# Kernel optimization log

Hardware: AMD Instinct MI355X
Metric: run time of the kernel (lower is better)

The kernel has to match this reference:

```python
import jax, jax.numpy as jnp
import numpy as np

# Grid / point-count constants (K-Radar-style sparse voxel grid)
B, Z, Y, X = 4, 40, 1024, 1024
Nr, Nl = 262144, 1048576
W_OCC, W_OFF, W_FEAT = 0.2, 1.0, 1.0
BIG = jnp.int32(1_000_000_000)  # sentinel for unmatched candidates


def _hash_zyx(b, z, y, x):
    # max value B*Z*Y*X ~ 1.7e8, fits int32
    return ((b * Z + z) * Y + y) * X + x


def _make_offsets(R):
    rng = np.arange(-R, R + 1)
    dz, dy, dx = np.meshgrid(rng, rng, rng, indexing='ij')
    return jnp.asarray(np.stack([dz.ravel(), dy.ravel(), dx.ravel()], axis=1), dtype=jnp.int32)  # [K,3]


def setup_inputs() -> dict:
    key = jax.random.key(0)
    k = jax.random.split(key, 10)
    radar_indices = jnp.stack([
        jax.random.randint(k[0], (Nr,), 0, B, dtype=jnp.int32),
        jax.random.randint(k[1], (Nr,), 0, Z, dtype=jnp.int32),
        jax.random.randint(k[2], (Nr,), 0, Y, dtype=jnp.int32),
        jax.random.randint(k[3], (Nr,), 0, X, dtype=jnp.int32)], axis=1)
    lidar_indices = jnp.stack([
        jax.random.randint(k[4], (Nl,), 0, B, dtype=jnp.int32),
        jax.random.randint(k[5], (Nl,), 0, Z, dtype=jnp.int32),
        jax.random.randint(k[6], (Nl,), 0, Y, dtype=jnp.int32),
        jax.random.randint(k[7], (Nl,), 0, X, dtype=jnp.int32)], axis=1)
    pred_feat = jax.random.normal(k[8], (Nr, 4), dtype=jnp.float32)
    pred_occ = jax.random.normal(k[9], (Nr, 1, 1), dtype=jnp.float32)
    lidar_features = jax.random.normal(jax.random.fold_in(key, 77), (Nl, 4), dtype=jnp.float32)
    return {"pred_feat": pred_feat, "pred_occ": pred_occ, "radar_indices": radar_indices,
            "lidar_features": lidar_features, "lidar_indices": lidar_indices, "R": 1}


def _local_match(radar_indices, lidar_indices, lidar_features, R):
    # Build sorted hash table of lidar voxels
    hL = _hash_zyx(lidar_indices[:, 0], lidar_indices[:, 1], lidar_indices[:, 2], lidar_indices[:, 3])
    ordL = jnp.argsort(hL)
    hL_sorted = hL[ordL]

    offs = _make_offsets(R)                      # [K,3]
    K = offs.shape[0]
    b, z, y, x = radar_indices[:, 0], radar_indices[:, 1], radar_indices[:, 2], radar_indices[:, 3]
    zz = jnp.clip(z[:, None] + offs[None, :, 0], 0, Z - 1)   # [Nr,K]
    yy = jnp.clip(y[:, None] + offs[None, :, 1], 0, Y - 1)
    xx = jnp.clip(x[:, None] + offs[None, :, 2], 0, X - 1)
    cand = _hash_zyx(b[:, None], zz, yy, xx).reshape(-1)      # [Nr*K]

    pos = jnp.searchsorted(hL_sorted, cand)                   # [Nr*K]
    safe_pos = jnp.clip(pos, 0, hL_sorted.shape[0] - 1)
    is_member = (pos < hL_sorted.shape[0]) & (hL_sorted[safe_pos] == cand)
    hit = is_member.reshape(-1, K)                            # [Nr,K]

    dL1 = jnp.sum(jnp.abs(offs), axis=1)                      # [K]
    dL1_masked = jnp.where(hit, dL1[None, :], BIG)            # [Nr,K]
    best_k = jnp.argmin(dL1_masked, axis=1)                   # [Nr]
    best = jnp.take_along_axis(dL1_masked, best_k[:, None], axis=1)[:, 0]
    matched = best < BIG                                      # [Nr] bool

    pos_flat = jnp.take_along_axis(pos.reshape(-1, K), best_k[:, None], axis=1)[:, 0]
    lidar_row = ordL[jnp.clip(pos_flat, 0, hL_sorted.shape[0] - 1)]
    gt_feat = jnp.where(matched[:, None], lidar_features[lidar_row], 0.0)  # [Nr, C_lidar]

    sel_z = jnp.take_along_axis(zz, best_k[:, None], axis=1)[:, 0]
    sel_y = jnp.take_along_axis(yy, best_k[:, None], axis=1)[:, 0]
    sel_x = jnp.take_along_axis(xx, best_k[:, None], axis=1)[:, 0]
    gt_offsets = jnp.stack([sel_z - z, sel_y - y, sel_x - x], axis=1).astype(jnp.float32)
    return matched, gt_offsets, gt_feat


def reference(pred_feat, pred_occ, radar_indices, lidar_features, lidar_indices, R):
    matched, gt_d, gt_f = _local_match(radar_indices, lidar_indices, lidar_features, R)
    gt_d = gt_d[:, ::-1]                              # torch.flip(gt_d, dims=[1])
    m = matched.astype(pred_feat.dtype)

    # BCEWithLogitsLoss(mean): logaddexp(0,x) - x*y
    occ_logits = jnp.mean(jnp.squeeze(pred_occ, axis=1), axis=-1)  # [Nr]
    occ_loss = jnp.mean(jnp.logaddexp(0.0, occ_logits) - occ_logits * m)

    cnt = jnp.sum(m)
    # smooth_l1 (beta=1, mean) over matched rows of pred offsets [M,3]
    diff = pred_feat[:, :3] - gt_d
    ad = jnp.abs(diff)
    sl1 = jnp.where(ad < 1.0, 0.5 * diff * diff, ad - 0.5)
    off_loss = jnp.sum(sl1 * m[:, None]) / jnp.maximum(cnt * 3.0, 1.0)
    # l1 (mean) over matched intensity column [M,1]
    feat_loss = jnp.sum(jnp.abs(pred_feat[:, 3:4] - gt_f[:, 3:4]) * m[:, None]) / jnp.maximum(cnt, 1.0)

    return W_OCC * occ_loss + W_OFF * off_loss + W_FEAT * feat_loss
```

## Files before the change

### kernel.cpp

```cpp
#include <hip/hip_runtime.h>
#include <math.h>
#include <limits.h>

#define BD 4
#define ZD 40
#define YD 1024
#define XD 1024
#define BZYX (167772160)

constexpr int BLOCK = 256;
constexpr unsigned SMALL_LOG = 19;
constexpr unsigned long long EMPTY64 = ~0ull;
constexpr size_t OCC_BYTES = (size_t)1 << (SMALL_LOG - 3);

typedef unsigned uvec4 __attribute__((ext_vector_type(4)));

__device__ __forceinline__ unsigned hash_mix(unsigned x) {
    x ^= x >> 16; x *= 0x7feb352dU;
    x ^= x >> 15; x *= 0x846ca68bU;
    x ^= x >> 16;
    return x;
}

__device__ __forceinline__ float smooth_l1(float d) {
    float ad = fabsf(d);
    return (ad < 1.0f) ? 0.5f * d * d : ad - 0.5f;
}

__device__ __forceinline__ float logaddexp0(float logit) {
    return (logit > 0.0f) ? (logit + log1pf(expf(-logit))) : log1pf(expf(logit));
}

__global__ void clear_bitmap(uvec4* __restrict__ bmv, int bmW4) {
    const uvec4 z = (uvec4)(0u);
    const int stride = gridDim.x * blockDim.x;
    for (int k = blockIdx.x * blockDim.x + threadIdx.x; k < bmW4; k += stride)
        bmv[k] = z;
}

__global__ void build_bitmap(const int4* __restrict__ li, int Nl,
                             unsigned* __restrict__ bm,
                             unsigned* __restrict__ cells,
                             uvec4* __restrict__ stv, int stW4) {
    const int gid = blockIdx.x * blockDim.x + threadIdx.x;
    if (gid < Nl) {
        int4 v = li[gid];
        unsigned cell = ((unsigned)(v.x * ZD + v.y) * YD + v.z) * XD + v.w;
        cells[gid] = cell;
        atomicOr(&bm[cell >> 5], 1u << (cell & 31));
    }
    const uvec4 f = (uvec4)(~0u);
    const int stride = gridDim.x * blockDim.x;
    for (int k = gid; k < stW4; k += stride)
        stv[k] = f;
}

__global__ void __launch_bounds__(BLOCK)
main_match(const float4* __restrict__ pf, const float* __restrict__ occ,
           const int4* __restrict__ ri, const unsigned* __restrict__ bm,
           unsigned long long* __restrict__ stab, unsigned* __restrict__ occbm,
           unsigned smask, const int* __restrict__ Rptr, int Nr,
           int* __restrict__ mcell, double* __restrict__ partials) {
    const int R = *Rptr;
    const int i = blockIdx.x * BLOCK + threadIdx.x;
    double occ_s = 0.0, cnt_s = 0.0, off_s = 0.0;

    if (i < Nr) {
        int4 rib = ri[i];
        const int b = rib.x, z = rib.y, y = rib.z, x = rib.w;
        int mc = -1;
        float m = 0.0f;
        int sx = 0, sy = 0, sz = 0;
        bool matched = false;

        if (R == 1) {
            const int xa = max(x - 1, 0);
            const int xc = min(x + 1, XD - 1);
            const int sa = x - xa;
            const int sc = xc - xa;
            unsigned hm = 0;
#pragma unroll
            for (int dz = -1; dz <= 1; ++dz) {
                const int zz = min(max(z + dz, 0), ZD - 1);
#pragma unroll
                for (int dy = -1; dy <= 1; ++dy) {
                    const int yy = min(max(y + dy, 0), YD - 1);
                    const unsigned n0 =
                        ((unsigned)(b * ZD + zz) * YD + yy) * XD + (unsigned)xa;
                    const unsigned q = n0 >> 5;
                    const int r = n0 & 31;
                    unsigned long long w =
                        ((unsigned long long)bm[q + 1] << 32) | bm[q];
                    w >>= r;
                    const int k0 = (dz + 1) * 9 + (dy + 1) * 3;
                    hm |= ((unsigned)(w & 1)) << (k0 + 0);
                    hm |= ((unsigned)((w >> sa) & 1)) << (k0 + 1);
                    hm |= ((unsigned)((w >> sc) & 1)) << (k0 + 2);
                }
            }
            const unsigned M0 = 1u << 13;
            const unsigned M1 = (1u << 4) | (1u << 10) | (1u << 12) |
                                (1u << 14) | (1u << 16) | (1u << 22);
            const unsigned M2 = (1u << 1) | (1u << 3) | (1u << 5) | (1u << 7) |
                                (1u << 9) | (1u << 11) | (1u << 15) | (1u << 17) |
                                (1u << 19) | (1u << 21) | (1u << 23) | (1u << 25);
            int bk = -1;
            if (hm & M0)       bk = 13;
            else if (hm & M1)  bk = __ffs((int)(hm & M1)) - 1;
            else if (hm & M2)  bk = __ffs((int)(hm & M2)) - 1;
            else if (hm)       bk = __ffs((int)hm) - 1;
            if (bk >= 0) {
                matched = true;
                const int dz = bk / 9 - 1, dy = (bk / 3) % 3 - 1, dx = bk % 3 - 1;
                sz = min(max(z + dz, 0), ZD - 1);
                sy = min(max(y + dy, 0), YD - 1);
                sx = min(max(x + dx, 0), XD - 1);
            }
        } else {
            int bestd = INT_MAX;
            for (int dz = -R; dz <= R; ++dz) {
                const int zz = min(max(z + dz, 0), ZD - 1);
                const int adz = abs(dz);
                for (int dy = -R; dy <= R; ++dy) {
                    const int yy = min(max(y + dy, 0), YD - 1);
                    const int adzy = adz + abs(dy);
                    for (int dx = -R; dx <= R; ++dx) {
                        const int d = adzy + abs(dx);
                        if (d >= bestd) continue;
                        const int xx = min(max(x + dx, 0), XD - 1);
                        const unsigned cell =
                            ((unsigned)(b * ZD + zz) * YD + yy) * XD + xx;
                        if ((bm[cell >> 5] >> (cell & 31)) & 1u) {
                            bestd = d; matched = true;
                            sz = zz; sy = yy; sx = xx;
                        }
                    }
                }
            }
        }

        if (matched) {
            m = 1.0f;
            cnt_s = 1.0;
            const unsigned cell = ((unsigned)(b * ZD + sz) * YD + sy) * XD + sx;
            mc = (int)cell;
            const float4 p = pf[i];
            off_s = (double)(smooth_l1(p.x - (float)(sx - x)) +
                             smooth_l1(p.y - (float)(sy - y)) +
                             smooth_l1(p.z - (float)(sz - z)));
            const unsigned long long desired =
                ((unsigned long long)cell << 32) | 0xFFFFFFFFull;
            unsigned s = hash_mix(cell) & smask;
            bool claimed = false;
            while (true) {
                unsigned long long old = atomicCAS(&stab[s], EMPTY64, desired);
                if (old == EMPTY64) { claimed = true; break; }
                if ((unsigned)(old >> 32) == cell) break;
                s = (s + 1) & smask;
            }
            if (claimed) atomicOr(&occbm[s >> 5], 1u << (s & 31));
        }
        mcell[i] = mc;
        const float logit = occ[i];
        occ_s = (double)(logaddexp0(logit) - logit * m);
    }

    __shared__ double sh[3][BLOCK];
    const int tid = threadIdx.x;
    sh[0][tid] = occ_s; sh[1][tid] = cnt_s; sh[2][tid] = off_s;
    __syncthreads();
    for (int s = BLOCK / 2; s > 0; s >>= 1) {
        if (tid < s) {
            sh[0][tid] += sh[0][tid + s];
            sh[1][tid] += sh[1][tid + s];
            sh[2][tid] += sh[2][tid + s];
        }
        __syncthreads();
    }
    if (tid == 0) {
        partials[blockIdx.x * 4 + 0] = sh[0][0];
        partials[blockIdx.x * 4 + 1] = sh[1][0];
        partials[blockIdx.x * 4 + 2] = sh[2][0];
        partials[blockIdx.x * 4 + 3] = 0.0;
    }
}

__global__ void lidar_scan(const unsigned* __restrict__ cells, int Nl,
                           unsigned long long* __restrict__ stab,
                           const unsigned* __restrict__ occbm, unsigned smask) {
    int j = blockIdx.x * blockDim.x + threadIdx.x;
    if (j >= Nl) return;
    const unsigned cell = cells[j];
    unsigned s = hash_mix(cell) & smask;
    if (!((occbm[s >> 5] >> (s & 31)) & 1u)) return;
    while (true) {
        const unsigned long long e = stab[s];
        if (e == EMPTY64) return;
        if ((unsigned)(e >> 32) == cell) {
            atomicMin((unsigned*)&stab[s], (unsigned)j);
            return;
        }
        s = (s + 1) & smask;
    }
}

__global__ void __launch_bounds__(BLOCK)
feat_pass(const float4* __restrict__ pf, const int* __restrict__ mcell,
          const unsigned long long* __restrict__ stab, unsigned smask,
          const float4* __restrict__ lf, int Nr, double* __restrict__ fpart) {
    const int i = blockIdx.x * BLOCK + threadIdx.x;
    double fs = 0.0;
    if (i < Nr) {
        const int mc = mcell[i];
        if (mc >= 0) {
            const unsigned cell = (unsigned)mc;
            unsigned s = hash_mix(cell) & smask;
            unsigned row = 0;
            while (true) {
                const unsigned long long e = stab[s];
                if ((unsigned)(e >> 32) == cell) { row = (unsigned)e; break; }
                s = (s + 1) & smask;
            }
            fs = (double)fabsf(pf[i].w - lf[row].w);
        }
    }
    __shared__ double sh[BLOCK];
    const int tid = threadIdx.x;
    sh[tid] = fs;
    __syncthreads();
    for (int s = BLOCK / 2; s > 0; s >>= 1) {
        if (tid < s) sh[tid] += sh[tid + s];
        __syncthreads();
    }
    if (tid == 0) fpart[blockIdx.x] = sh[0];
}


__global__ void fb_insert(const int4* __restrict__ li, int Nl,
                          unsigned long long* __restrict__ tab, unsigned cmask) {
    int i = blockIdx.x * blockDim.x + threadIdx.x;
    if (i >= Nl) return;
    int4 v = li[i];
    const unsigned cell = ((unsigned)(v.x * ZD + v.y) * YD + v.z) * XD + v.w;
    const unsigned long long desired = ((unsigned long long)cell << 32) | (unsigned)i;
    unsigned s = hash_mix(cell) & cmask;
    unsigned probes = 0;
    while (probes++ <= cmask) {
        const unsigned long long old = atomicCAS(&tab[s], EMPTY64, desired);
        if (old == EMPTY64) return;
        if ((unsigned)(old >> 32) == cell) {
            atomicMin((unsigned*)&tab[s], (unsigned)i);
            return;
        }
        s = (s + 1) & cmask;
    }
}

__global__ void __launch_bounds__(BLOCK)
fb_main(const float4* __restrict__ pf, const float* __restrict__ occ,
        const int4* __restrict__ ri, const float4* __restrict__ lf,
        const unsigned long long* __restrict__ tab, unsigned cmask,
        const int* __restrict__ Rptr, int Nr, double* __restrict__ partials) {
    const int R = *Rptr;
    const int i = blockIdx.x * BLOCK + threadIdx.x;
    double occ_s = 0.0, cnt_s = 0.0, off_s = 0.0, feat_s = 0.0;
    if (i < Nr) {
        int4 rib = ri[i];
        const int b = rib.x, z = rib.y, y = rib.z, x = rib.w;
        int bestd = INT_MAX, bestRow = -1;
        int sx = 0, sy = 0, sz = 0;
        for (int dz = -R; dz <= R; ++dz) {
            const int zz = min(max(z + dz, 0), ZD - 1);
            const int adz = abs(dz);
            for (int dy = -R; dy <= R; ++dy) {
                const int yy = min(max(y + dy, 0), YD - 1);
                const int adzy = adz + abs(dy);
                for (int dx = -R; dx <= R; ++dx) {
                    const int d = adzy + abs(dx);
                    if (d >= bestd) continue;
                    const int xx = min(max(x + dx, 0), XD - 1);
                    const unsigned cell =
                        ((unsigned)(b * ZD + zz) * YD + yy) * XD + xx;
                    unsigned s = hash_mix(cell) & cmask;
                    int row = -1;
                    while (true) {
                        const unsigned long long e = tab[s];
                        if ((unsigned)(e >> 32) == cell) { row = (int)(unsigned)e; break; }
                        if (e == EMPTY64) break;
                        s = (s + 1) & cmask;
                    }
                    if (row >= 0) { bestd = d; bestRow = row; sz = zz; sy = yy; sx = xx; }
                }
            }
        }
        const float m = (bestRow >= 0) ? 1.0f : 0.0f;
        const float logit = occ[i];
        occ_s = (double)(logaddexp0(logit) - logit * m);
        if (bestRow >= 0) {
            cnt_s = 1.0;
            const float4 p = pf[i];
            off_s = (double)(smooth_l1(p.x - (float)(sx - x)) +
                             smooth_l1(p.y - (float)(sy - y)) +
                             smooth_l1(p.z - (float)(sz - z)));
            feat_s = (double)fabsf(p.w - lf[bestRow].w);
        }
    }
    __shared__ double sh[4][BLOCK];
    const int tid = threadIdx.x;
    sh[0][tid] = occ_s; sh[1][tid] = cnt_s; sh[2][tid] = off_s; sh[3][tid] = feat_s;
    __syncthreads();
    for (int s = BLOCK / 2; s > 0; s >>= 1) {
        if (tid < s) {
            sh[0][tid] += sh[0][tid + s];
            sh[1][tid] += sh[1][tid + s];
            sh[2][tid] += sh[2][tid + s];
            sh[3][tid] += sh[3][tid + s];
        }
        __syncthreads();
    }
    if (tid == 0) {
        partials[blockIdx.x * 4 + 0] = sh[0][0];
        partials[blockIdx.x * 4 + 1] = sh[1][0];
        partials[blockIdx.x * 4 + 2] = sh[2][0];
        partials[blockIdx.x * 4 + 3] = sh[3][0];
    }
}


__global__ void finalize_kernel(const double* __restrict__ partials,
                                const double* __restrict__ fpart, int nblk,
                                int Nr, float* __restrict__ out) {
    __shared__ double sh[4][BLOCK];
    const int tid = threadIdx.x;
    double a0 = 0, a1 = 0, a2 = 0, a3 = 0;
    for (int i = tid; i < nblk; i += BLOCK) {
        a0 += partials[i * 4 + 0];
        a1 += partials[i * 4 + 1];
        a2 += partials[i * 4 + 2];
        a3 += partials[i * 4 + 3] + fpart[i];
    }
    sh[0][tid] = a0; sh[1][tid] = a1; sh[2][tid] = a2; sh[3][tid] = a3;
    __syncthreads();
    for (int s = BLOCK / 2; s > 0; s >>= 1) {
        if (tid < s) {
            sh[0][tid] += sh[0][tid + s];
            sh[1][tid] += sh[1][tid + s];
            sh[2][tid] += sh[2][tid + s];
            sh[3][tid] += sh[3][tid + s];
        }
        __syncthreads();
    }
    if (tid == 0) {
        const double occ_loss = sh[0][0] / (double)Nr;
        const double cnt = sh[1][0];
        const double off_loss = sh[2][0] / fmax(cnt * 3.0, 1.0);
        const double feat_loss = sh[3][0] / fmax(cnt, 1.0);
        out[0] = (float)(0.2 * occ_loss + 1.0 * off_loss + 1.0 * feat_loss);
    }
}

extern "C" void kernel_launch(void* const* d_in, const int* in_sizes, int n_in,
                              void* d_out, int out_size, void* d_ws, size_t ws_size,
                              hipStream_t stream) {
    const float* pred_feat  = (const float*)d_in[0];
    const float* pred_occ   = (const float*)d_in[1];
    const int*   radar_idx  = (const int*)d_in[2];
    const float* lidar_feat = (const float*)d_in[3];
    const int*   lidar_idx  = (const int*)d_in[4];
    const int*   Rptr       = (const int*)d_in[5];

    const int Nr = in_sizes[0] / 4;
    const int Nl = in_sizes[3] / 4;
    const int nblk  = (Nr + BLOCK - 1) / BLOCK;
    const int nblkL = (Nl + BLOCK - 1) / BLOCK;

    size_t off = 0;
    auto alloc = [&](size_t n) { size_t o = off; off += (n + 255) & ~(size_t)255; return o; };
    const size_t bmBytes   = (size_t)BZYX / 8 + 64;
    const size_t stabBytes = (size_t)8 << SMALL_LOG;
    const size_t bmOff   = alloc(bmBytes);
    const size_t occOff  = alloc(OCC_BYTES);
    const size_t clearEnd = off;
    const size_t stabOff = alloc(stabBytes);
    const size_t cellOff = alloc((size_t)Nl * 4);
    const size_t mcOff   = alloc((size_t)Nr * 4);
    const size_t pOff    = alloc((size_t)nblk * 4 * sizeof(double));
    const size_t fpOff   = alloc((size_t)nblk * sizeof(double));
    const size_t needD = off;

    char* ws = (char*)d_ws;
    if (needD <= ws_size) {
        unsigned*           bm    = (unsigned*)(ws + bmOff);
        unsigned*           occbm = (unsigned*)(ws + occOff);
        unsigned long long* stab  = (unsigned long long*)(ws + stabOff);
        unsigned*           cells = (unsigned*)(ws + cellOff);
        int*                mcell = (int*)(ws + mcOff);
        double*             parts = (double*)(ws + pOff);
        double*             fpart = (double*)(ws + fpOff);
        const unsigned smask = (1u << SMALL_LOG) - 1;
        const int stW4 = (int)(stabBytes / 16);

        clear_bitmap<<<4096, BLOCK, 0, stream>>>((uvec4*)ws, (int)(clearEnd / 16));
        build_bitmap<<<nblkL, BLOCK, 0, stream>>>(
            (const int4*)lidar_idx, Nl, bm, cells, (uvec4*)stab, stW4);
        main_match<<<nblk, BLOCK, 0, stream>>>(
            (const float4*)pred_feat, pred_occ, (const int4*)radar_idx,
            bm, stab, occbm, smask, Rptr, Nr, mcell, parts);
        lidar_scan<<<nblkL, BLOCK, 0, stream>>>(cells, Nl, stab, occbm, smask);
        feat_pass<<<nblk, BLOCK, 0, stream>>>(
            (const float4*)pred_feat, mcell, stab, smask,
            (const float4*)lidar_feat, Nr, fpart);
        finalize_kernel<<<1, BLOCK, 0, stream>>>(parts, fpart, nblk, Nr, (float*)d_out);
    } else {
        const size_t tailBytes = (size_t)nblk * 5 * sizeof(double) + 512;
        unsigned C = 1u << 22;
        while ((size_t)C * 8 + tailBytes > ws_size && C > (1u << 21)) C >>= 1;
        const unsigned cmask = C - 1;
        unsigned long long* tab = (unsigned long long*)ws;
        double* parts = (double*)(ws + ((size_t)C * 8 + 255 & ~(size_t)255));
        double* fpart = parts + (size_t)nblk * 4;

        hipError_t e1 = hipMemsetAsync(tab, 0xFF, (size_t)C * 8, stream); (void)e1;
        hipError_t e2 = hipMemsetAsync(fpart, 0x00, (size_t)nblk * sizeof(double), stream); (void)e2;

        fb_insert<<<nblkL, BLOCK, 0, stream>>>((const int4*)lidar_idx, Nl, tab, cmask);
        fb_main<<<nblk, BLOCK, 0, stream>>>(
            (const float4*)pred_feat, pred_occ, (const int4*)radar_idx,
            (const float4*)lidar_feat, tab, cmask, Rptr, Nr, parts);
        finalize_kernel<<<1, BLOCK, 0, stream>>>(parts, fpart, nblk, Nr, (float*)d_out);
    }
}
```

Before: 114.3 us.

## Partition bitmap build by XCD slice so atomics stay L2-local

The lidar bitmap build now assigns each block to one of eight bitmap slices, chosen from the block index modulo 8, which is meant to match how blocks are spread round-robin across the MI355X's XCDs. Every slice's blocks read all lidar points but only issue atomicOr for words inside their own slice. The aim is to keep each bitmap word's atomics inside one XCD's L2 and avoid cross-die coherence traffic. The cost is that the lidar index array is read eight times, using nontemporal loads, and the grid is fixed at 2048 blocks.

```diff
diff --git a/kernel.cpp b/kernel.cpp
--- a/kernel.cpp
+++ b/kernel.cpp
@@ -14,6 +14,7 @@
 constexpr size_t OCC_BYTES = (size_t)1 << (SMALL_LOG - 3);
 
 typedef unsigned uvec4 __attribute__((ext_vector_type(4)));
+typedef int      ivec4 __attribute__((ext_vector_type(4)));
 
 __device__ __forceinline__ unsigned hash_mix(unsigned x) {
     x ^= x >> 16; x *= 0x7feb352dU;
@@ -38,20 +39,27 @@
         bmv[k] = z;
 }
 
-__global__ void build_bitmap(const int4* __restrict__ li, int Nl,
-                             unsigned* __restrict__ bm,
-                             unsigned* __restrict__ cells,
-                             uvec4* __restrict__ stv, int stW4) {
-    const int gid = blockIdx.x * blockDim.x + threadIdx.x;
-    if (gid < Nl) {
-        int4 v = li[gid];
-        unsigned cell = ((unsigned)(v.x * ZD + v.y) * YD + v.z) * XD + v.w;
-        cells[gid] = cell;
-        atomicOr(&bm[cell >> 5], 1u << (cell & 31));
+__global__ void __launch_bounds__(BLOCK)
+build_xcd(const ivec4* __restrict__ li, int Nl,
+          unsigned* __restrict__ bm, unsigned sliceWords,
+          unsigned* __restrict__ cells,
+          uvec4* __restrict__ stv, int stW4) {
+    const unsigned slice = blockIdx.x & 7u;
+    const unsigned wlo = slice * sliceWords;
+    const unsigned whi = wlo + sliceWords;
+    const int chunk = blockIdx.x >> 3;
+    const int nch = (int)(gridDim.x >> 3);
+    const int stridePts = nch * BLOCK;
+    for (int j = chunk * BLOCK + threadIdx.x; j < Nl; j += stridePts) {
+        const ivec4 v = __builtin_nontemporal_load(&li[j]);
+        const unsigned cell = ((unsigned)(v.x * ZD + v.y) * YD + v.z) * XD + (unsigned)v.w;
+        if (slice == 0) cells[j] = cell;
+        const unsigned w = cell >> 5;
+        if (w >= wlo && w < whi) atomicOr(&bm[w], 1u << (cell & 31));
     }
     const uvec4 f = (uvec4)(~0u);
-    const int stride = gridDim.x * blockDim.x;
-    for (int k = gid; k < stW4; k += stride)
+    const int stride = (int)(gridDim.x * blockDim.x);
+    for (int k = blockIdx.x * blockDim.x + threadIdx.x; k < stW4; k += stride)
         stv[k] = f;
 }
 
@@ -399,10 +407,11 @@
         double*             fpart = (double*)(ws + fpOff);
         const unsigned smask = (1u << SMALL_LOG) - 1;
         const int stW4 = (int)(stabBytes / 16);
+        const unsigned sliceWords = (unsigned)((BZYX / 32) / 8);
 
         clear_bitmap<<<4096, BLOCK, 0, stream>>>((uvec4*)ws, (int)(clearEnd / 16));
-        build_bitmap<<<nblkL, BLOCK, 0, stream>>>(
-            (const int4*)lidar_idx, Nl, bm, cells, (uvec4*)stab, stW4);
+        build_xcd<<<2048, BLOCK, 0, stream>>>(
+            (const ivec4*)lidar_idx, Nl, bm, sliceWords, cells, (uvec4*)stab, stW4);
         main_match<<<nblk, BLOCK, 0, stream>>>(
             (const float4*)pred_feat, pred_occ, (const int4*)radar_idx,
             bm, stab, occbm, smask, Rptr, Nr, mcell, parts);
```

Measured after the change: 121.0 us. 1.06x slower.

## Build lidar occupancy bitmap via binned shared-memory pass instead of global clear plus atomics

Applied to the files above, without the earlier changes.

Replaces the full 21MB bitmap clear and scattered global atomicOr with a two-phase build: lidar cells are first bucketed into 1024 contiguous bitmap ranges, then each block assembles its range in shared memory and writes it out with dense vector stores. An overflow list handles bins exceeding capacity. This removes the separate global memset and random atomics, but adds an extra binning pass, workspace for bins, and two more kernel launches.

```diff
diff --git a/kernel.cpp b/kernel.cpp
--- a/kernel.cpp
+++ b/kernel.cpp
@@ -13,7 +13,12 @@
 constexpr unsigned long long EMPTY64 = ~0ull;
 constexpr size_t OCC_BYTES = (size_t)1 << (SMALL_LOG - 3);
 
+constexpr int NBINS = 1024;
+constexpr unsigned WORDS_PER_BIN = (unsigned)((BZYX / 32) / NBINS);
+constexpr int BINCAP = 3072;
+
 typedef unsigned uvec4 __attribute__((ext_vector_type(4)));
+typedef int      ivec4 __attribute__((ext_vector_type(4)));
 
 __device__ __forceinline__ unsigned hash_mix(unsigned x) {
     x ^= x >> 16; x *= 0x7feb352dU;
@@ -31,28 +36,59 @@
     return (logit > 0.0f) ? (logit + log1pf(expf(-logit))) : log1pf(expf(logit));
 }
 
-__global__ void clear_bitmap(uvec4* __restrict__ bmv, int bmW4) {
+__global__ void clear_small(uvec4* __restrict__ v, int n4) {
     const uvec4 z = (uvec4)(0u);
     const int stride = gridDim.x * blockDim.x;
-    for (int k = blockIdx.x * blockDim.x + threadIdx.x; k < bmW4; k += stride)
-        bmv[k] = z;
-}
-
-__global__ void build_bitmap(const int4* __restrict__ li, int Nl,
-                             unsigned* __restrict__ bm,
-                             unsigned* __restrict__ cells,
-                             uvec4* __restrict__ stv, int stW4) {
-    const int gid = blockIdx.x * blockDim.x + threadIdx.x;
-    if (gid < Nl) {
-        int4 v = li[gid];
-        unsigned cell = ((unsigned)(v.x * ZD + v.y) * YD + v.z) * XD + v.w;
-        cells[gid] = cell;
-        atomicOr(&bm[cell >> 5], 1u << (cell & 31));
-    }
+    for (int k = blockIdx.x * blockDim.x + threadIdx.x; k < n4; k += stride)
+        v[k] = z;
+}
+
+__global__ void __launch_bounds__(BLOCK)
+k_bin(const ivec4* __restrict__ li, int Nl, unsigned* __restrict__ cells,
+      unsigned* __restrict__ bins, unsigned* __restrict__ bcnt,
+      unsigned* __restrict__ ovf, unsigned* __restrict__ ovfcnt) {
+    const int j = blockIdx.x * BLOCK + threadIdx.x;
+    if (j >= Nl) return;
+    const ivec4 v = __builtin_nontemporal_load(&li[j]);
+    const unsigned cell = ((unsigned)(v.x * ZD + v.y) * YD + v.z) * XD + (unsigned)v.w;
+    cells[j] = cell;
+    const unsigned bin = (cell >> 5) / WORDS_PER_BIN;
+    const unsigned off = atomicAdd(&bcnt[bin], 1u);
+    if (off < (unsigned)BINCAP) bins[(size_t)bin * BINCAP + off] = cell;
+    else { const unsigned o = atomicAdd(ovfcnt, 1u); ovf[o] = cell; }
+}
+
+__global__ void __launch_bounds__(BLOCK)
+k_bits(const unsigned* __restrict__ bins, const unsigned* __restrict__ bcnt,
+       unsigned* __restrict__ bm, uvec4* __restrict__ stv, int stW4) {
+    extern __shared__ unsigned lbm[];
+    const int bin = blockIdx.x;
+    const int tid = threadIdx.x;
+    for (unsigned w = tid; w < WORDS_PER_BIN; w += BLOCK) lbm[w] = 0u;
+    __syncthreads();
+    const unsigned n = min(bcnt[bin], (unsigned)BINCAP);
+    const unsigned base = (unsigned)bin * WORDS_PER_BIN;
+    for (unsigned k = tid; k < n; k += BLOCK) {
+        const unsigned cell = bins[(size_t)bin * BINCAP + k];
+        atomicOr(&lbm[(cell >> 5) - base], 1u << (cell & 31));
+    }
+    __syncthreads();
+    uvec4* dst = (uvec4*)(bm + base);
+    const uvec4* src = (const uvec4*)lbm;
+    for (unsigned w4 = tid; w4 < WORDS_PER_BIN / 4; w4 += BLOCK)
+        dst[w4] = src[w4];
     const uvec4 f = (uvec4)(~0u);
-    const int stride = gridDim.x * blockDim.x;
-    for (int k = gid; k < stW4; k += stride)
+    for (int k = blockIdx.x * BLOCK + tid; k < stW4; k += (int)(gridDim.x * BLOCK))
         stv[k] = f;
+}
+
+__global__ void k_ovf(const unsigned* __restrict__ ovf,
+                      const unsigned* __restrict__ ovfcnt,
+                      unsigned* __restrict__ bm) {
+    const unsigned n = *ovfcnt;
+    const unsigned stride = gridDim.x * blockDim.x;
+    for (unsigned k = blockIdx.x * blockDim.x + threadIdx.x; k < n; k += stride)
+        atomicOr(&bm[ovf[k] >> 5], 1u << (ovf[k] & 31));
 }
 
 __global__ void __launch_bounds__(BLOCK)
@@ -376,14 +412,19 @@
 
     size_t off = 0;
     auto alloc = [&](size_t n) { size_t o = off; off += (n + 255) & ~(size_t)255; return o; };
-    const size_t bmBytes   = (size_t)BZYX / 8 + 64;
+    const size_t bmBytes   = (size_t)BZYX / 8;
     const size_t stabBytes = (size_t)8 << SMALL_LOG;
     const size_t bmOff   = alloc(bmBytes);
+    const size_t padOff  = alloc(256);
     const size_t occOff  = alloc(OCC_BYTES);
+    const size_t bcntOff = alloc((size_t)NBINS * 4);
+    const size_t ovcOff  = alloc(256);
     const size_t clearEnd = off;
     const size_t stabOff = alloc(stabBytes);
     const size_t cellOff = alloc((size_t)Nl * 4);
     const size_t mcOff   = alloc((size_t)Nr * 4);
+    const size_t binOff  = alloc((size_t)NBINS * BINCAP * 4);
+    const size_t ovfOff  = alloc((size_t)Nl * 4);
     const size_t pOff    = alloc((size_t)nblk * 4 * sizeof(double));
     const size_t fpOff   = alloc((size_t)nblk * sizeof(double));
     const size_t needD = off;
@@ -392,17 +433,26 @@
     if (needD <= ws_size) {
         unsigned*           bm    = (unsigned*)(ws + bmOff);
         unsigned*           occbm = (unsigned*)(ws + occOff);
+        unsigned*           bcnt  = (unsigned*)(ws + bcntOff);
+        unsigned*           ovfc  = (unsigned*)(ws + ovcOff);
         unsigned long long* stab  = (unsigned long long*)(ws + stabOff);
         unsigned*           cells = (unsigned*)(ws + cellOff);
         int*                mcell = (int*)(ws + mcOff);
+        unsigned*           bins  = (unsigned*)(ws + binOff);
+        unsigned*           ovf   = (unsigned*)(ws + ovfOff);
         double*             parts = (double*)(ws + pOff);
         double*             fpart = (double*)(ws + fpOff);
         const unsigned smask = (1u << SMALL_LOG) - 1;
         const int stW4 = (int)(stabBytes / 16);
-
-        clear_bitmap<<<4096, BLOCK, 0, stream>>>((uvec4*)ws, (int)(clearEnd / 16));
-        build_bitmap<<<nblkL, BLOCK, 0, stream>>>(
-            (const int4*)lidar_idx, Nl, bm, cells, (uvec4*)stab, stW4);
+        const size_t clearBytes = clearEnd - padOff;
+
+        clear_small<<<64, BLOCK, 0, stream>>>(
+            (uvec4*)(ws + padOff), (int)(clearBytes / 16));
+        k_bin<<<nblkL, BLOCK, 0, stream>>>(
+            (const ivec4*)lidar_idx, Nl, cells, bins, bcnt, ovf, ovfc);
+        k_bits<<<NBINS, BLOCK, WORDS_PER_BIN * 4, stream>>>(
+            bins, bcnt, bm, (uvec4*)stab, stW4);
+        k_ovf<<<64, BLOCK, 0, stream>>>(ovf, ovfc, bm);
         main_match<<<nblk, BLOCK, 0, stream>>>(
             (const float4*)pred_feat, pred_occ, (const int4*)radar_idx,
             bm, stab, occbm, smask, Rptr, Nr, mcell, parts);
```

Result: slower. 289.0 us (+152.9%).
